# Kernel optimization log

Measured on AMD Instinct MI355X. Metric: run time of the kernel, lower is better.

Reference implementation:

```python
import jax, jax.numpy as jnp
import numpy as np

B, N = 128, 1369
DINO, CLIP, H = 384, 512, 8
D = CLIP // H  # head_dim = 64
EPS = 1e-5


def setup_inputs() -> dict:
    key = jax.random.key(0)
    ks = jax.random.split(key, 8)
    s_clip = 1.0 / np.sqrt(CLIP)
    s_dino = 1.0 / np.sqrt(DINO)
    return {
        "dino_features": jax.random.normal(ks[0], (B, N, DINO), jnp.float32),
        "clip_features": jax.random.normal(ks[1], (B, CLIP), jnp.float32),
        "Wq": jax.random.uniform(ks[2], (CLIP, CLIP), jnp.float32, -s_clip, s_clip),
        "bq": jnp.zeros((CLIP,), jnp.float32),
        "Wk": jax.random.uniform(ks[3], (DINO, CLIP), jnp.float32, -s_dino, s_dino),
        "bk": jnp.zeros((CLIP,), jnp.float32),
        "Wv": jax.random.uniform(ks[4], (DINO, CLIP), jnp.float32, -s_dino, s_dino),
        "bv": jnp.zeros((CLIP,), jnp.float32),
        "temperature": jnp.ones((1,), jnp.float32),
        "ln_gamma": jnp.ones((CLIP,), jnp.float32),
        "ln_beta": jnp.zeros((CLIP,), jnp.float32),
    }


def reference(dino_features, clip_features, Wq, bq, Wk, bk, Wv, bv,
              temperature, ln_gamma, ln_beta):
    # Q: (B, H, D) -- single query token from CLIP
    Q = (clip_features @ Wq + bq).reshape(B, H, D)
    # K, V: (B, N, H, D)
    K = (dino_features @ Wk + bk).reshape(B, N, H, D)
    V = (dino_features @ Wv + bv).reshape(B, N, H, D)
    scale = jnp.sqrt(jnp.float32(D)) * temperature[0]
    # attention logits over patches: (B, H, N)
    logits = jnp.einsum("bhd,bnhd->bhn", Q, K) / scale
    attn = jax.nn.softmax(logits, axis=-1)  # dropout is identity in eval mode
    out = jnp.einsum("bhn,bnhd->bhd", attn, V).reshape(B, CLIP)
    # LayerNorm over last dim
    mu = out.mean(axis=-1, keepdims=True)
    var = out.var(axis=-1, keepdims=True)
    return (out - mu) * jax.lax.rsqrt(var + EPS) * ln_gamma + ln_beta
```

## Files before the change

### kernel.cpp

```cpp
#include <hip/hip_runtime.h>
#include <math.h>

#define B_    128
#define N_    1369
#define DINO_ 384
#define CLIP_ 512
#define H_    8
#define CHUNKS 6
#define CH     229

__device__ __forceinline__ float wave_sum(float v) {
  v += __shfl_xor(v, 1);  v += __shfl_xor(v, 2);  v += __shfl_xor(v, 4);
  v += __shfl_xor(v, 8);  v += __shfl_xor(v, 16); v += __shfl_xor(v, 32);
  return v;
}

__device__ __forceinline__ float fold8(const float* v, int lane) {
  float a0, a1, a2, a3;
  {
    float t0 = __shfl_xor(v[0], 32), t1 = __shfl_xor(v[1], 32);
    float t2 = __shfl_xor(v[2], 32), t3 = __shfl_xor(v[3], 32);
    float u0 = __shfl_xor(v[4], 32), u1 = __shfl_xor(v[5], 32);
    float u2 = __shfl_xor(v[6], 32), u3 = __shfl_xor(v[7], 32);
    const bool hi = (lane & 32) != 0;
    a0 = hi ? v[4] + u0 : v[0] + t0;
    a1 = hi ? v[5] + u1 : v[1] + t1;
    a2 = hi ? v[6] + u2 : v[2] + t2;
    a3 = hi ? v[7] + u3 : v[3] + t3;
  }
  float b0, b1;
  {
    float t0 = __shfl_xor(a0, 16), t1 = __shfl_xor(a1, 16);
    float t2 = __shfl_xor(a2, 16), t3 = __shfl_xor(a3, 16);
    const bool hi = (lane & 16) != 0;
    b0 = hi ? a2 + t2 : a0 + t0;
    b1 = hi ? a3 + t3 : a1 + t1;
  }
  float c0;
  {
    float t0 = __shfl_xor(b0, 8), t1 = __shfl_xor(b1, 8);
    const bool hi = (lane & 8) != 0;
    c0 = hi ? b1 + t1 : b0 + t0;
  }
  c0 += __shfl_xor(c0, 4);
  c0 += __shfl_xor(c0, 2);
  c0 += __shfl_xor(c0, 1);
  return c0;
}

__device__ __forceinline__ void bcast8(float p, float* P) {
  P[0] = p;
  P[1] = __shfl_xor(P[0], 8);
  P[2] = __shfl_xor(P[0], 16);
  P[3] = __shfl_xor(P[1], 16);
  P[4] = __shfl_xor(P[0], 32);
  P[5] = __shfl_xor(P[1], 32);
  P[6] = __shfl_xor(P[2], 32);
  P[7] = __shfl_xor(P[3], 32);
}

__global__ __launch_bounds__(256) void kq(const float* __restrict__ clip,
                                          const float* __restrict__ Wq,
                                          const float* __restrict__ bq,
                                          float* __restrict__ Q) {
  const int b = blockIdx.x;
  const int c = blockIdx.y * 256 + threadIdx.x;
  __shared__ float cl[CLIP_];
  cl[threadIdx.x] = clip[b * CLIP_ + threadIdx.x];
  cl[threadIdx.x + 256] = clip[b * CLIP_ + threadIdx.x + 256];
  __syncthreads();
  float acc = bq[c];
  #pragma unroll 8
  for (int j = 0; j < CLIP_; ++j) acc += cl[j] * Wq[j * CLIP_ + c];
  Q[b * CLIP_ + c] = acc;
}

__global__ __launch_bounds__(256) void kt(const float* __restrict__ Wk,
                                          float* __restrict__ WkT) {
  __shared__ float tile[64][65];
  const int tx = threadIdx.x & 63, ty = threadIdx.x >> 6;
  const int c0 = blockIdx.x * 64, j0 = blockIdx.y * 64;
  #pragma unroll
  for (int k = 0; k < 16; ++k) {
    const int jj = ty + 4 * k;
    tile[jj][tx] = Wk[(j0 + jj) * CLIP_ + c0 + tx];
  }
  __syncthreads();
  #pragma unroll
  for (int k = 0; k < 16; ++k) {
    const int cc = ty + 4 * k;
    WkT[(size_t)(c0 + cc) * DINO_ + j0 + tx] = tile[tx][cc];
  }
}

__global__ __launch_bounds__(256) void kqk(const float* __restrict__ WkT,
                                           const float* __restrict__ Q,
                                           const float* __restrict__ temp,
                                           float* __restrict__ qkout) {
  const int b = blockIdx.x;
  const int e = blockIdx.y * 256 + threadIdx.x;
  __shared__ float qs[CLIP_];
  qs[threadIdx.x] = Q[b * CLIP_ + threadIdx.x];
  qs[threadIdx.x + 256] = Q[b * CLIP_ + threadIdx.x + 256];
  __syncthreads();
  const int h = e / DINO_;
  const int j = e - h * DINO_;
  const float rs = 1.0f / (8.0f * temp[0]);
  float acc = 0.0f;
  #pragma unroll 8
  for (int d = 0; d < 64; ++d)
    acc += WkT[(size_t)(h * 64 + d) * DINO_ + j] * qs[h * 64 + d];
  qkout[(size_t)b * 3072 + e] = acc * rs;
}

__global__ __launch_bounds__(256, 3) void kmain(const float* __restrict__ dino,
                                                const float* __restrict__ qk,
                                                float* __restrict__ ps,
                                                float* __restrict__ pl) {
  const int blk = blockIdx.x;
  const int b = blk / CHUNKS;
  const int c = blk - b * CHUNKS;
  const int n0 = c * CH;
  const int n1 = min(N_, n0 + CH);
  const int tid = threadIdx.x, w = tid >> 6, lane = tid & 63;
  const int phi = (((lane >> 5) & 1) << 2) | (((lane >> 4) & 1) << 1) | ((lane >> 3) & 1);

  float qr[H_][6];
  const float* qkb = qk + (size_t)b * 3072;
  #pragma unroll
  for (int h = 0; h < H_; ++h)
    #pragma unroll
    for (int i = 0; i < 3; ++i) {
      const float2 t = *(const float2*)(qkb + h * DINO_ + i * 128 + 2 * lane);
      qr[h][2 * i] = t.x;  qr[h][2 * i + 1] = t.y;
    }

  float s[H_][6];
  float l = 0.0f;
  #pragma unroll
  for (int j = 0; j < H_; ++j)
    #pragma unroll
    for (int k = 0; k < 6; ++k) s[j][k] = 0.0f;

  const float* dbase = dino + (size_t)b * N_ * DINO_;

  for (int n = n0 + w; n < n1; n += 8) {
    const int n2 = n + 4;
    const bool hb = n2 < n1;
    const float* ra = dbase + (size_t)n * DINO_;
    const float* rb = dbase + (size_t)(hb ? n2 : n) * DINO_;
    float2 xa[3], xb[3];
    #pragma unroll
    for (int i = 0; i < 3; ++i) xa[i] = *(const float2*)(ra + i * 128 + 2 * lane);
    #pragma unroll
    for (int i = 0; i < 3; ++i) xb[i] = *(const float2*)(rb + i * 128 + 2 * lane);

    float va[H_];
    #pragma unroll
    for (int h = 0; h < H_; ++h)
      va[h] = qr[h][0] * xa[0].x + qr[h][1] * xa[0].y + qr[h][2] * xa[1].x
            + qr[h][3] * xa[1].y + qr[h][4] * xa[2].x + qr[h][5] * xa[2].y;
    float vb[H_];
    #pragma unroll
    for (int h = 0; h < H_; ++h)
      vb[h] = qr[h][0] * xb[0].x + qr[h][1] * xb[0].y + qr[h][2] * xb[1].x
            + qr[h][3] * xb[1].y + qr[h][4] * xb[2].x + qr[h][5] * xb[2].y;

    const float pa = __expf(fold8(va, lane));
    const float pb = __expf(fold8(vb, lane));
    float Pa[H_], Pb[H_];
    bcast8(pa, Pa);
    bcast8(pb, Pb);

    l += pa;
    #pragma unroll
    for (int j = 0; j < H_; ++j) {
      s[j][0] += Pa[j] * xa[0].x;  s[j][1] += Pa[j] * xa[0].y;
      s[j][2] += Pa[j] * xa[1].x;  s[j][3] += Pa[j] * xa[1].y;
      s[j][4] += Pa[j] * xa[2].x;  s[j][5] += Pa[j] * xa[2].y;
    }
    if (hb) {
      l += pb;
      #pragma unroll
      for (int j = 0; j < H_; ++j) {
        s[j][0] += Pb[j] * xb[0].x;  s[j][1] += Pb[j] * xb[0].y;
        s[j][2] += Pb[j] * xb[1].x;  s[j][3] += Pb[j] * xb[1].y;
        s[j][4] += Pb[j] * xb[2].x;  s[j][5] += Pb[j] * xb[2].y;
      }
    }
  }

  __shared__ float sm[2][3072];
  __shared__ float lm[2][H_];
  if (w >= 2) {
    #pragma unroll
    for (int j = 0; j < H_; ++j)
      #pragma unroll
      for (int k = 0; k < 6; ++k)
        sm[w - 2][(phi ^ j) * DINO_ + (k >> 1) * 128 + 2 * lane + (k & 1)] = s[j][k];
    if ((lane & 7) == 0) lm[w - 2][phi] = l;
  }
  __syncthreads();
  if (w < 2) {
    #pragma unroll
    for (int j = 0; j < H_; ++j)
      #pragma unroll
      for (int k = 0; k < 6; ++k)
        s[j][k] += sm[w][(phi ^ j) * DINO_ + (k >> 1) * 128 + 2 * lane + (k & 1)];
    if ((lane & 7) == 0) l += lm[w][phi];
  }
  __syncthreads();
  if (w == 1) {
    #pragma unroll
    for (int j = 0; j < H_; ++j)
      #pragma unroll
      for (int k = 0; k < 6; ++k)
        sm[0][(phi ^ j) * DINO_ + (k >> 1) * 128 + 2 * lane + (k & 1)] = s[j][k];
    if ((lane & 7) == 0) lm[0][phi] = l;
  }
  __syncthreads();
  if (w == 0) {
    #pragma unroll
    for (int j = 0; j < H_; ++j)
      #pragma unroll
      for (int k = 0; k < 6; ++k)
        s[j][k] += sm[0][(phi ^ j) * DINO_ + (k >> 1) * 128 + 2 * lane + (k & 1)];
    if ((lane & 7) == 0) l += lm[0][phi];
    float* pso = ps + (size_t)blk * 3072;
    #pragma unroll
    for (int j = 0; j < H_; ++j)
      #pragma unroll
      for (int k = 0; k < 6; ++k)
        pso[(phi ^ j) * DINO_ + (k >> 1) * 128 + 2 * lane + (k & 1)] = s[j][k];
    if ((lane & 7) == 0) pl[blk * H_ + phi] = l;
  }
}

__global__ __launch_bounds__(256) void km(const float* __restrict__ ps,
                                          const float* __restrict__ pl,
                                          float* __restrict__ sf) {
  const int b = blockIdx.x, tid = threadIdx.x;
  __shared__ float rL[H_];
  if (tid < H_) {
    float L = 0.0f;
    #pragma unroll
    for (int cc = 0; cc < CHUNKS; ++cc) L += pl[(b * CHUNKS + cc) * H_ + tid];
    rL[tid] = 1.0f / L;
  }
  __syncthreads();
  #pragma unroll
  for (int r = 0; r < 12; ++r) {
    const int e = tid + 256 * r;
    float acc = 0.0f;
    #pragma unroll
    for (int cc = 0; cc < CHUNKS; ++cc)
      acc += ps[(size_t)(b * CHUNKS + cc) * 3072 + e];
    sf[(size_t)b * 3072 + e] = acc * rL[e / DINO_];
  }
}

__global__ __launch_bounds__(512) void kf(const float* __restrict__ sf,
                                          const float* __restrict__ Wv,
                                          const float* __restrict__ bv,
                                          const float* __restrict__ gamma,
                                          const float* __restrict__ beta,
                                          float* __restrict__ out) {
  const int b = blockIdx.x, tid = threadIdx.x;
  const int w = tid >> 6, lane = tid & 63;
  __shared__ float sfl[3072];
  #pragma unroll
  for (int k = 0; k < 6; ++k) sfl[tid + 512 * k] = sf[(size_t)b * 3072 + tid + 512 * k];
  __syncthreads();
  const float* srow = sfl + (tid >> 6) * DINO_;
  float acc = bv[tid];
  #pragma unroll 8
  for (int d = 0; d < DINO_; ++d) acc += srow[d] * Wv[d * CLIP_ + tid];
  float sum = wave_sum(acc);
  float sq  = wave_sum(acc * acc);
  __shared__ float rS[8], rQ[8];
  if (lane == 0) { rS[w] = sum; rQ[w] = sq; }
  __syncthreads();
  float tot = 0.0f, totq = 0.0f;
  #pragma unroll
  for (int i = 0; i < 8; ++i) { tot += rS[i]; totq += rQ[i]; }
  const float mu = tot * (1.0f / 512.0f);
  const float var = totq * (1.0f / 512.0f) - mu * mu;
  const float rstd = rsqrtf(var + 1e-5f);
  out[(size_t)b * CLIP_ + tid] = (acc - mu) * rstd * gamma[tid] + beta[tid];
}

extern "C" void kernel_launch(void* const* d_in, const int* in_sizes, int n_in,
                              void* d_out, int out_size, void* d_ws, size_t ws_size,
                              hipStream_t stream) {
  const float* dino  = (const float*)d_in[0];
  const float* clip  = (const float*)d_in[1];
  const float* Wq    = (const float*)d_in[2];
  const float* bq    = (const float*)d_in[3];
  const float* Wk    = (const float*)d_in[4];
  const float* Wv    = (const float*)d_in[6];
  const float* bv    = (const float*)d_in[7];
  const float* temp  = (const float*)d_in[8];
  const float* gamma = (const float*)d_in[9];
  const float* beta  = (const float*)d_in[10];
  float* out = (float*)d_out;

  float* ws  = (float*)d_ws;
  float* Q   = ws;
  float* WkT = Q   + 65536;
  float* qk  = WkT + 196608;
  float* ps  = qk  + 393216;
  float* pl  = ps  + 2359296;
  float* sf  = pl  + 6144;

  kq  <<<dim3(B_, 2),  256, 0, stream>>>(clip, Wq, bq, Q);
  kt  <<<dim3(8, 6),   256, 0, stream>>>(Wk, WkT);
  kqk <<<dim3(B_, 12), 256, 0, stream>>>(WkT, Q, temp, qk);
  kmain<<<B_ * CHUNKS, 256, 0, stream>>>(dino, qk, ps, pl);
  km  <<<B_,           256, 0, stream>>>(ps, pl, sf);
  kf  <<<B_,           512, 0, stream>>>(sf, Wv, bv, gamma, beta, out);
}
```

Baseline: 470.3 us.

## Split attention into single-wave chunks and fuse front and back kernels

The main kernel now uses one 64-thread wave per block over 24 sequence chunks per batch, which removes the in-block shared-memory reduction and gives many more independent blocks. The Q projection and Q·Wk folding are merged into one kernel, and the partial-sum merge is fused with the Wv projection and LayerNorm. Loads are widened to float4+float2 per lane. The trade-off is four times more partial sums written to and read back from global memory.

```diff
diff --git a/kernel.cpp b/kernel.cpp
--- a/kernel.cpp
+++ b/kernel.cpp
@@ -6,8 +6,8 @@
 #define DINO_ 384
 #define CLIP_ 512
 #define H_    8
-#define CHUNKS 6
-#define CH     229
+#define CHUNKS 24
+#define CH     58
 
 __device__ __forceinline__ float wave_sum(float v) {
   v += __shfl_xor(v, 1);  v += __shfl_xor(v, 2);  v += __shfl_xor(v, 4);
@@ -59,22 +59,6 @@
   P[7] = __shfl_xor(P[3], 32);
 }
 
-__global__ __launch_bounds__(256) void kq(const float* __restrict__ clip,
-                                          const float* __restrict__ Wq,
-                                          const float* __restrict__ bq,
-                                          float* __restrict__ Q) {
-  const int b = blockIdx.x;
-  const int c = blockIdx.y * 256 + threadIdx.x;
-  __shared__ float cl[CLIP_];
-  cl[threadIdx.x] = clip[b * CLIP_ + threadIdx.x];
-  cl[threadIdx.x + 256] = clip[b * CLIP_ + threadIdx.x + 256];
-  __syncthreads();
-  float acc = bq[c];
-  #pragma unroll 8
-  for (int j = 0; j < CLIP_; ++j) acc += cl[j] * Wq[j * CLIP_ + c];
-  Q[b * CLIP_ + c] = acc;
-}
-
 __global__ __launch_bounds__(256) void kt(const float* __restrict__ Wk,
                                           float* __restrict__ WkT) {
   __shared__ float tile[64][65];
@@ -93,47 +77,57 @@
   }
 }
 
-__global__ __launch_bounds__(256) void kqk(const float* __restrict__ WkT,
-                                           const float* __restrict__ Q,
-                                           const float* __restrict__ temp,
-                                           float* __restrict__ qkout) {
-  const int b = blockIdx.x;
-  const int e = blockIdx.y * 256 + threadIdx.x;
+__global__ __launch_bounds__(512) void kfront(const float* __restrict__ clip,
+                                              const float* __restrict__ Wq,
+                                              const float* __restrict__ bq,
+                                              const float* __restrict__ WkT,
+                                              const float* __restrict__ temp,
+                                              float* __restrict__ qkout) {
+  const int b = blockIdx.x, tid = threadIdx.x;
+  __shared__ float cl[CLIP_];
   __shared__ float qs[CLIP_];
-  qs[threadIdx.x] = Q[b * CLIP_ + threadIdx.x];
-  qs[threadIdx.x + 256] = Q[b * CLIP_ + threadIdx.x + 256];
-  __syncthreads();
-  const int h = e / DINO_;
-  const int j = e - h * DINO_;
+  cl[tid] = clip[b * CLIP_ + tid];
+  __syncthreads();
+  float acc = bq[tid];
+  #pragma unroll 8
+  for (int j = 0; j < CLIP_; ++j) acc += cl[j] * Wq[j * CLIP_ + tid];
+  qs[tid] = acc;
+  __syncthreads();
   const float rs = 1.0f / (8.0f * temp[0]);
-  float acc = 0.0f;
-  #pragma unroll 8
-  for (int d = 0; d < 64; ++d)
-    acc += WkT[(size_t)(h * 64 + d) * DINO_ + j] * qs[h * 64 + d];
-  qkout[(size_t)b * 3072 + e] = acc * rs;
-}
-
-__global__ __launch_bounds__(256, 3) void kmain(const float* __restrict__ dino,
-                                                const float* __restrict__ qk,
-                                                float* __restrict__ ps,
-                                                float* __restrict__ pl) {
+  #pragma unroll
+  for (int r = 0; r < 6; ++r) {
+    const int e = tid + 512 * r;
+    const int h = e / DINO_;
+    const int j = e - h * DINO_;
+    float a2 = 0.0f;
+    #pragma unroll 8
+    for (int d = 0; d < 64; ++d)
+      a2 += WkT[(size_t)(h * 64 + d) * DINO_ + j] * qs[h * 64 + d];
+    qkout[(size_t)b * 3072 + e] = a2 * rs;
+  }
+}
+
+__global__ __launch_bounds__(64, 3) void kmain(const float* __restrict__ dino,
+                                               const float* __restrict__ qk,
+                                               float* __restrict__ ps,
+                                               float* __restrict__ pl) {
   const int blk = blockIdx.x;
   const int b = blk / CHUNKS;
   const int c = blk - b * CHUNKS;
   const int n0 = c * CH;
   const int n1 = min(N_, n0 + CH);
-  const int tid = threadIdx.x, w = tid >> 6, lane = tid & 63;
+  const int lane = threadIdx.x;
   const int phi = (((lane >> 5) & 1) << 2) | (((lane >> 4) & 1) << 1) | ((lane >> 3) & 1);
 
   float qr[H_][6];
   const float* qkb = qk + (size_t)b * 3072;
   #pragma unroll
-  for (int h = 0; h < H_; ++h)
-    #pragma unroll
-    for (int i = 0; i < 3; ++i) {
-      const float2 t = *(const float2*)(qkb + h * DINO_ + i * 128 + 2 * lane);
-      qr[h][2 * i] = t.x;  qr[h][2 * i + 1] = t.y;
-    }
+  for (int h = 0; h < H_; ++h) {
+    const float4 t4 = *(const float4*)(qkb + h * DINO_ + 4 * lane);
+    const float2 t2 = *(const float2*)(qkb + h * DINO_ + 256 + 2 * lane);
+    qr[h][0] = t4.x; qr[h][1] = t4.y; qr[h][2] = t4.z; qr[h][3] = t4.w;
+    qr[h][4] = t2.x; qr[h][5] = t2.y;
+  }
 
   float s[H_][6];
   float l = 0.0f;
@@ -144,137 +138,77 @@
 
   const float* dbase = dino + (size_t)b * N_ * DINO_;
 
-  for (int n = n0 + w; n < n1; n += 8) {
-    const int n2 = n + 4;
-    const bool hb = n2 < n1;
-    const float* ra = dbase + (size_t)n * DINO_;
-    const float* rb = dbase + (size_t)(hb ? n2 : n) * DINO_;
-    float2 xa[3], xb[3];
-    #pragma unroll
-    for (int i = 0; i < 3; ++i) xa[i] = *(const float2*)(ra + i * 128 + 2 * lane);
-    #pragma unroll
-    for (int i = 0; i < 3; ++i) xb[i] = *(const float2*)(rb + i * 128 + 2 * lane);
-
-    float va[H_];
+  for (int n = n0; n < n1; ++n) {
+    const float* row = dbase + (size_t)n * DINO_;
+    const float4 x4 = *(const float4*)(row + 4 * lane);
+    const float2 x2 = *(const float2*)(row + 256 + 2 * lane);
+    float v[H_];
     #pragma unroll
     for (int h = 0; h < H_; ++h)
-      va[h] = qr[h][0] * xa[0].x + qr[h][1] * xa[0].y + qr[h][2] * xa[1].x
-            + qr[h][3] * xa[1].y + qr[h][4] * xa[2].x + qr[h][5] * xa[2].y;
-    float vb[H_];
-    #pragma unroll
-    for (int h = 0; h < H_; ++h)
-      vb[h] = qr[h][0] * xb[0].x + qr[h][1] * xb[0].y + qr[h][2] * xb[1].x
-            + qr[h][3] * xb[1].y + qr[h][4] * xb[2].x + qr[h][5] * xb[2].y;
-
-    const float pa = __expf(fold8(va, lane));
-    const float pb = __expf(fold8(vb, lane));
-    float Pa[H_], Pb[H_];
-    bcast8(pa, Pa);
-    bcast8(pb, Pb);
-
-    l += pa;
+      v[h] = qr[h][0] * x4.x + qr[h][1] * x4.y + qr[h][2] * x4.z
+           + qr[h][3] * x4.w + qr[h][4] * x2.x + qr[h][5] * x2.y;
+    const float p = __expf(fold8(v, lane));
+    float P[H_];
+    bcast8(p, P);
+    l += p;
     #pragma unroll
     for (int j = 0; j < H_; ++j) {
-      s[j][0] += Pa[j] * xa[0].x;  s[j][1] += Pa[j] * xa[0].y;
-      s[j][2] += Pa[j] * xa[1].x;  s[j][3] += Pa[j] * xa[1].y;
-      s[j][4] += Pa[j] * xa[2].x;  s[j][5] += Pa[j] * xa[2].y;
+      s[j][0] += P[j] * x4.x;  s[j][1] += P[j] * x4.y;
+      s[j][2] += P[j] * x4.z;  s[j][3] += P[j] * x4.w;
+      s[j][4] += P[j] * x2.x;  s[j][5] += P[j] * x2.y;
     }
-    if (hb) {
-      l += pb;
-      #pragma unroll
-      for (int j = 0; j < H_; ++j) {
-        s[j][0] += Pb[j] * xb[0].x;  s[j][1] += Pb[j] * xb[0].y;
-        s[j][2] += Pb[j] * xb[1].x;  s[j][3] += Pb[j] * xb[1].y;
-        s[j][4] += Pb[j] * xb[2].x;  s[j][5] += Pb[j] * xb[2].y;
-      }
-    }
-  }
-
-  __shared__ float sm[2][3072];
-  __shared__ float lm[2][H_];
-  if (w >= 2) {
-    #pragma unroll
-    for (int j = 0; j < H_; ++j)
-      #pragma unroll
-      for (int k = 0; k < 6; ++k)
-        sm[w - 2][(phi ^ j) * DINO_ + (k >> 1) * 128 + 2 * lane + (k & 1)] = s[j][k];
-    if ((lane & 7) == 0) lm[w - 2][phi] = l;
-  }
-  __syncthreads();
-  if (w < 2) {
-    #pragma unroll
-    for (int j = 0; j < H_; ++j)
-      #pragma unroll
-      for (int k = 0; k < 6; ++k)
-        s[j][k] += sm[w][(phi ^ j) * DINO_ + (k >> 1) * 128 + 2 * lane + (k & 1)];
-    if ((lane & 7) == 0) l += lm[w][phi];
-  }
-  __syncthreads();
-  if (w == 1) {
-    #pragma unroll
-    for (int j = 0; j < H_; ++j)
-      #pragma unroll
-      for (int k = 0; k < 6; ++k)
-        sm[0][(phi ^ j) * DINO_ + (k >> 1) * 128 + 2 * lane + (k & 1)] = s[j][k];
-    if ((lane & 7) == 0) lm[0][phi] = l;
-  }
-  __syncthreads();
-  if (w == 0) {
-    #pragma unroll
-    for (int j = 0; j < H_; ++j)
-      #pragma unroll
-      for (int k = 0; k < 6; ++k)
-        s[j][k] += sm[0][(phi ^ j) * DINO_ + (k >> 1) * 128 + 2 * lane + (k & 1)];
-    if ((lane & 7) == 0) l += lm[0][phi];
-    float* pso = ps + (size_t)blk * 3072;
-    #pragma unroll
-    for (int j = 0; j < H_; ++j)
-      #pragma unroll
-      for (int k = 0; k < 6; ++k)
-        pso[(phi ^ j) * DINO_ + (k >> 1) * 128 + 2 * lane + (k & 1)] = s[j][k];
-    if ((lane & 7) == 0) pl[blk * H_ + phi] = l;
-  }
-}
-
-__global__ __launch_bounds__(256) void km(const float* __restrict__ ps,
-                                          const float* __restrict__ pl,
-                                          float* __restrict__ sf) {
-  const int b = blockIdx.x, tid = threadIdx.x;
-  __shared__ float rL[H_];
-  if (tid < H_) {
-    float L = 0.0f;
-    #pragma unroll
-    for (int cc = 0; cc < CHUNKS; ++cc) L += pl[(b * CHUNKS + cc) * H_ + tid];
-    rL[tid] = 1.0f / L;
-  }
-  __syncthreads();
-  #pragma unroll
-  for (int r = 0; r < 12; ++r) {
-    const int e = tid + 256 * r;
-    float acc = 0.0f;
-    #pragma unroll
-    for (int cc = 0; cc < CHUNKS; ++cc)
-      acc += ps[(size_t)(b * CHUNKS + cc) * 3072 + e];
-    sf[(size_t)b * 3072 + e] = acc * rL[e / DINO_];
-  }
-}
-
-__global__ __launch_bounds__(512) void kf(const float* __restrict__ sf,
-                                          const float* __restrict__ Wv,
-                                          const float* __restrict__ bv,
-                                          const float* __restrict__ gamma,
-                                          const float* __restrict__ beta,
-                                          float* __restrict__ out) {
+  }
+
+  float* pso = ps + (size_t)blk * 3072;
+  #pragma unroll
+  for (int j = 0; j < H_; ++j) {
+    const int hh = phi ^ j;
+    *(float4*)(pso + hh * DINO_ + 4 * lane) = make_float4(s[j][0], s[j][1], s[j][2], s[j][3]);
+    *(float2*)(pso + hh * DINO_ + 256 + 2 * lane) = make_float2(s[j][4], s[j][5]);
+  }
+  if ((lane & 7) == 0) pl[blk * H_ + phi] = l;
+}
+
+__global__ __launch_bounds__(512) void kback(const float* __restrict__ ps,
+                                             const float* __restrict__ pl,
+                                             const float* __restrict__ Wv,
+                                             const float* __restrict__ bv,
+                                             const float* __restrict__ gamma,
+                                             const float* __restrict__ beta,
+                                             float* __restrict__ out) {
   const int b = blockIdx.x, tid = threadIdx.x;
   const int w = tid >> 6, lane = tid & 63;
   __shared__ float sfl[3072];
-  #pragma unroll
-  for (int k = 0; k < 6; ++k) sfl[tid + 512 * k] = sf[(size_t)b * 3072 + tid + 512 * k];
-  __syncthreads();
+  __shared__ float rL[H_];
+
+  float acc6[6];
+  #pragma unroll
+  for (int k = 0; k < 6; ++k) acc6[k] = 0.0f;
+  const float* pb = ps + (size_t)b * CHUNKS * 3072;
+  for (int cc = 0; cc < CHUNKS; ++cc) {
+    #pragma unroll
+    for (int k = 0; k < 6; ++k)
+      acc6[k] += pb[(size_t)cc * 3072 + tid + 512 * k];
+  }
+  if (tid < H_) {
+    float L = 0.0f;
+    #pragma unroll
+    for (int cc = 0; cc < CHUNKS; ++cc) L += pl[(b * CHUNKS + cc) * H_ + tid];
+    rL[tid] = 1.0f / L;
+  }
+  __syncthreads();
+  #pragma unroll
+  for (int k = 0; k < 6; ++k) {
+    const int e = tid + 512 * k;
+    sfl[e] = acc6[k] * rL[e / DINO_];
+  }
+  __syncthreads();
+
   const float* srow = sfl + (tid >> 6) * DINO_;
   float acc = bv[tid];
   #pragma unroll 8
   for (int d = 0; d < DINO_; ++d) acc += srow[d] * Wv[d * CLIP_ + tid];
+
   float sum = wave_sum(acc);
   float sq  = wave_sum(acc * acc);
   __shared__ float rS[8], rQ[8];
@@ -305,17 +239,13 @@
   float* out = (float*)d_out;
 
   float* ws  = (float*)d_ws;
-  float* Q   = ws;
-  float* WkT = Q   + 65536;
+  float* WkT = ws;
   float* qk  = WkT + 196608;
   float* ps  = qk  + 393216;
-  float* pl  = ps  + 2359296;
-  float* sf  = pl  + 6144;
-
-  kq  <<<dim3(B_, 2),  256, 0, stream>>>(clip, Wq, bq, Q);
-  kt  <<<dim3(8, 6),   256, 0, stream>>>(Wk, WkT);
-  kqk <<<dim3(B_, 12), 256, 0, stream>>>(WkT, Q, temp, qk);
-  kmain<<<B_ * CHUNKS, 256, 0, stream>>>(dino, qk, ps, pl);
-  km  <<<B_,           256, 0, stream>>>(ps, pl, sf);
-  kf  <<<B_,           512, 0, stream>>>(sf, Wv, bv, gamma, beta, out);
-}
+  float* pl  = ps  + 9437184;
+
+  kt    <<<dim3(8, 6),   256, 0, stream>>>(Wk, WkT);
+  kfront<<<B_,           512, 0, stream>>>(clip, Wq, bq, WkT, temp, qk);
+  kmain <<<B_ * CHUNKS,  64,  0, stream>>>(dino, qk, ps, pl);
+  kback <<<B_,           512, 0, stream>>>(ps, pl, Wv, bv, gamma, beta, out);
+}
```

Result: slower. 480.1 us (+2.1%).
